# Kernel optimization log

Measured on AMD Instinct MI355X. Metric: run time of the kernel, lower is better.

## Reference

```python
import jax, jax.numpy as jnp
import numpy as np

D_MODEL = 1024
HEADS = 16
HEAD_DIM = D_MODEL // HEADS


def setup_inputs() -> dict:
    key = jax.random.key(0)
    ks = jax.random.split(key, 11)
    B, S = 2, 2048
    scale = 1.0 / np.sqrt(D_MODEL)
    inp = {
        "Q": jax.random.normal(ks[0], (B, S, D_MODEL), jnp.float32),
        "K": jax.random.normal(ks[1], (B, S, D_MODEL), jnp.float32),
        "V": jax.random.normal(ks[2], (B, S, D_MODEL), jnp.float32),
        "Wq": jax.random.normal(ks[3], (D_MODEL, D_MODEL), jnp.float32) * scale,
        "bq": jnp.zeros((D_MODEL,), jnp.float32),
        "Wk": jax.random.normal(ks[4], (D_MODEL, D_MODEL), jnp.float32) * scale,
        "bk": jnp.zeros((D_MODEL,), jnp.float32),
        "Wv": jax.random.normal(ks[5], (D_MODEL, D_MODEL), jnp.float32) * scale,
        "bv": jnp.zeros((D_MODEL,), jnp.float32),
        "Wo": jax.random.normal(ks[6], (D_MODEL, D_MODEL), jnp.float32) * scale,
        "bo": jnp.zeros((D_MODEL,), jnp.float32),
    }
    return inp


def reference(Q, K, V, Wq, bq, Wk, bk, Wv, bv, Wo, bo):
    B, S, _ = Q.shape
    # Linear projections (nn.Linear: x @ W^T + b), split into heads: [B, H, S, Dh]
    def proj(x, W, b):
        y = x @ W.T + b
        return y.reshape(B, S, HEADS, HEAD_DIM).transpose(0, 2, 1, 3)

    q = proj(Q, Wq, bq)
    k = proj(K, Wk, bk)
    v = proj(V, Wv, bv)

    # Scaled dot-product attention (dropout is identity in eval / p=0)
    scores = jnp.einsum("bhqd,bhkd->bhqk", q, k) / jnp.sqrt(
        jnp.asarray(HEAD_DIM, q.dtype)
    )
    weights = jax.nn.softmax(scores, axis=-1)
    ctx = jnp.einsum("bhqk,bhkd->bhqd", weights, v)  # [B, H, S, Dh]

    # Concatenate heads and output projection
    concat = ctx.transpose(0, 2, 1, 3).reshape(B, S, D_MODEL)
    return concat @ Wo.T + bo
```

## Files before the change

kernel.cpp:

```cpp
#include <hip/hip_runtime.h>
#include <hip/hip_bf16.h>

#define D_MODEL 1024
#define HEADS 16
#define HDIM 64
#define BATCH 2
#define SEQ 2048
#define MROWS (BATCH*SEQ)

typedef __attribute__((ext_vector_type(8))) short bf16x8;
typedef __attribute__((ext_vector_type(4))) float f32x4;
typedef __attribute__((ext_vector_type(16))) float f32x16;
typedef __attribute__((ext_vector_type(4))) float float4v;
typedef __attribute__((ext_vector_type(4))) unsigned u32x4;
typedef __attribute__((ext_vector_type(4))) short s16x4;

typedef const __attribute__((address_space(1))) void gconst_t;
typedef __attribute__((address_space(3))) void lds_t;
#define GLD16(g, l) __builtin_amdgcn_global_load_lds((gconst_t*)(g), (lds_t*)(l), 16, 0, 0)

__device__ __forceinline__ unsigned short f2b(float f) {
  unsigned u = __builtin_bit_cast(unsigned, f);
  u += 0x7fffu + ((u >> 16) & 1u);
  return (unsigned short)(u >> 16);
}

__device__ __forceinline__ unsigned cvtpk(float lo, float hi) {
  unsigned r;
  asm volatile("v_cvt_pk_bf16_f32 %0, %1, %2" : "=v"(r) : "v"(lo), "v"(hi));
  return r;
}

__global__ __launch_bounds__(256)
void cast_all(const float* __restrict__ Q, const float* __restrict__ K,
              const float* __restrict__ V, const float* __restrict__ Wq,
              const float* __restrict__ Wk, const float* __restrict__ Wv,
              const float* __restrict__ Wo, char* __restrict__ ws)
{
  const size_t MB = 1024*1024;
  int b = blockIdx.x;
  const float* src; short* dst; int rb;
  if (b < 6144) {
    int t = b >> 11; rb = b & 2047;
    src = (t == 0) ? Q : (t == 1) ? K : V;
    dst = (short*)(ws + (size_t)t*8*MB);
  } else {
    int t = (b - 6144) >> 9; rb = (b - 6144) & 511;
    src = (t == 0) ? Wq : (t == 1) ? Wk : (t == 2) ? Wv : Wo;
    dst = (short*)(ws + (24 + 2*(size_t)t)*MB);
  }
  int i = rb*256 + threadIdx.x;
  const float4v* s = (const float4v*)src;
  float4v a = s[2*(size_t)i], c = s[2*(size_t)i + 1];
  bf16x8 o;
  o[0] = (short)f2b(a[0]); o[1] = (short)f2b(a[1]);
  o[2] = (short)f2b(a[2]); o[3] = (short)f2b(a[3]);
  o[4] = (short)f2b(c[0]); o[5] = (short)f2b(c[1]);
  o[6] = (short)f2b(c[2]); o[7] = (short)f2b(c[3]);
  *(bf16x8*)(dst + 8*(size_t)i) = o;
}

__global__ __launch_bounds__(256)
void gemm_qkv(const short* __restrict__ Qb, const short* __restrict__ Kb,
              const short* __restrict__ Vb, const short* __restrict__ Wqb,
              const short* __restrict__ Wkb, const short* __restrict__ Wvb,
              const float* __restrict__ bq, const float* __restrict__ bk,
              const float* __restrict__ bv, short* __restrict__ qp,
              short* __restrict__ kp, short* __restrict__ vp)
{
  __shared__ __align__(16) short smem[128*129];
  short* lA = smem;
  short* lB = smem + 128*32;
  short* lT = smem;

  const int z = blockIdx.z;
  const short* A = (z == 0) ? Qb : (z == 1) ? Kb : Vb;
  const short* W = (z == 0) ? Wqb : (z == 1) ? Wkb : Wvb;
  const float* bias = (z == 0) ? bq : (z == 1) ? bk : bv;

  const int tid  = threadIdx.x;
  const int wid  = tid >> 6;
  const int lane = tid & 63;
  const int bm = blockIdx.x, bn = blockIdx.y;
  const int wr = wid >> 1, wc = wid & 1;

  f32x4 acc[4][4] = {};

  const int srow = tid >> 2;
  const int sseg = (tid & 3) * 8;
  const short* gA = A + (size_t)(bm*128 + srow)*D_MODEL + sseg;
  const short* gB = W + (size_t)(bn*128 + srow)*D_MODEL + sseg;
  short* lA0 = &lA[(wid*16)*32];
  short* lA1 = &lA[(64 + wid*16)*32];
  short* lB0 = &lB[(wid*16)*32];
  short* lB1 = &lB[(64 + wid*16)*32];

  const int fro  = lane & 15;
  const int koff = (lane >> 4) * 8;

  for (int kt = 0; kt < D_MODEL/32; ++kt) {
    const int ko = kt*32;
    GLD16(gA + ko,               lA0);
    GLD16(gA + 64*D_MODEL + ko,  lA1);
    GLD16(gB + ko,               lB0);
    GLD16(gB + 64*D_MODEL + ko,  lB1);
    __syncthreads();
    bf16x8 af[4], bfv[4];
    #pragma unroll
    for (int i = 0; i < 4; ++i)
      af[i] = *(const bf16x8*)&lA[(wr*64 + i*16 + fro)*32 + koff];
    #pragma unroll
    for (int j = 0; j < 4; ++j)
      bfv[j] = *(const bf16x8*)&lB[(wc*64 + j*16 + fro)*32 + koff];
    #pragma unroll
    for (int i = 0; i < 4; ++i)
      #pragma unroll
      for (int j = 0; j < 4; ++j)
        acc[i][j] = __builtin_amdgcn_mfma_f32_16x16x32_bf16(af[i], bfv[j], acc[i][j], 0, 0, 0);
    __syncthreads();
  }

  if (z < 2) {
    const float sc = (z == 0) ? 0.125f*1.44269504f : 1.0f;
    short* out = (z == 0) ? qp : kp;
    #pragma unroll
    for (int i = 0; i < 4; ++i) {
      #pragma unroll
      for (int r = 0; r < 4; ++r) {
        const int m = bm*128 + wr*64 + i*16 + (lane>>4)*4 + r;
        const int b = m >> 11, s = m & (SEQ-1);
        #pragma unroll
        for (int j = 0; j < 4; ++j) {
          const int n = bn*128 + wc*64 + j*16 + fro;
          const int h = n >> 6, dh = n & 63;
          float v = (acc[i][j][r] + bias[n]) * sc;
          out[((size_t)(b*HEADS + h)*SEQ + s)*HDIM + dh] = (short)f2b(v);
        }
      }
    }
  } else {
    #pragma unroll
    for (int i = 0; i < 4; ++i) {
      #pragma unroll
      for (int r = 0; r < 4; ++r) {
        const int ml = wr*64 + i*16 + (lane>>4)*4 + r;
        #pragma unroll
        for (int j = 0; j < 4; ++j) {
          const int nl = wc*64 + j*16 + fro;
          lT[nl*129 + ml] = (short)f2b(acc[i][j][r] + bias[bn*128 + nl]);
        }
      }
    }
    __syncthreads();
    const int nl = tid >> 1, mh = (tid & 1) * 64;
    const int n = bn*128 + nl, h = n >> 6, dh = n & 63;
    const int b  = (bm*128) >> 11;
    const int s0 = (bm*128) & (SEQ-1);
    const size_t base = ((size_t)(b*HEADS + h)*HDIM + dh)*SEQ + s0 + mh;
    #pragma unroll
    for (int v8 = 0; v8 < 8; ++v8) {
      bf16x8 vv;
      #pragma unroll
      for (int e = 0; e < 8; ++e) vv[e] = lT[nl*129 + mh + v8*8 + e];
      *(bf16x8*)&vp[base + v8*8] = vv;
    }
  }
}

__global__ __launch_bounds__(256)
void gemm_out(const short* __restrict__ A, const short* __restrict__ W,
              const float* __restrict__ bias, float* __restrict__ out)
{
  __shared__ __align__(16) short lA[128*32];
  __shared__ __align__(16) short lB[128*32];

  const int tid  = threadIdx.x;
  const int wid  = tid >> 6;
  const int lane = tid & 63;
  const int bm = blockIdx.x, bn = blockIdx.y;
  const int wr = wid >> 1, wc = wid & 1;

  f32x4 acc[4][4] = {};
  const int srow = tid >> 2;
  const int sseg = (tid & 3) * 8;
  const short* gA = A + (size_t)(bm*128 + srow)*D_MODEL + sseg;
  const short* gB = W + (size_t)(bn*128 + srow)*D_MODEL + sseg;
  short* lA0 = &lA[(wid*16)*32];
  short* lA1 = &lA[(64 + wid*16)*32];
  short* lB0 = &lB[(wid*16)*32];
  short* lB1 = &lB[(64 + wid*16)*32];
  const int fro  = lane & 15;
  const int koff = (lane >> 4) * 8;

  for (int kt = 0; kt < D_MODEL/32; ++kt) {
    const int ko = kt*32;
    GLD16(gA + ko,               lA0);
    GLD16(gA + 64*D_MODEL + ko,  lA1);
    GLD16(gB + ko,               lB0);
    GLD16(gB + 64*D_MODEL + ko,  lB1);
    __syncthreads();
    bf16x8 af[4], bfv[4];
    #pragma unroll
    for (int i = 0; i < 4; ++i)
      af[i] = *(const bf16x8*)&lA[(wr*64 + i*16 + fro)*32 + koff];
    #pragma unroll
    for (int j = 0; j < 4; ++j)
      bfv[j] = *(const bf16x8*)&lB[(wc*64 + j*16 + fro)*32 + koff];
    #pragma unroll
    for (int i = 0; i < 4; ++i)
      #pragma unroll
      for (int j = 0; j < 4; ++j)
        acc[i][j] = __builtin_amdgcn_mfma_f32_16x16x32_bf16(af[i], bfv[j], acc[i][j], 0, 0, 0);
    __syncthreads();
  }

  #pragma unroll
  for (int i = 0; i < 4; ++i) {
    #pragma unroll
    for (int r = 0; r < 4; ++r) {
      const int m = bm*128 + wr*64 + i*16 + (lane>>4)*4 + r;
      #pragma unroll
      for (int j = 0; j < 4; ++j) {
        const int n = bn*128 + wc*64 + j*16 + fro;
        out[(size_t)m*D_MODEL + n] = acc[i][j][r] + bias[n];
      }
    }
  }
}

__global__ __launch_bounds__(512)
void attn(const short* __restrict__ qws, const short* __restrict__ kws,
          const short* __restrict__ vws, short* __restrict__ ctx)
{
  __shared__ __align__(16) short lK[2][2][64*64];
  __shared__ __align__(16) short lV[2][2][64*64];

  const int tid = threadIdx.x, wid = tid >> 6, lane = tid & 63;
  const int sw = wid & 3, half = wid >> 2;
  const int bid = blockIdx.x;
  const int wg = (bid & 7) * 64 + (bid >> 3);
  const int qt = wg & 15, bh = wg >> 4;
  const size_t hb = (size_t)bh * SEQ * HDIM;

  const int lane31 = lane & 31, hi = lane >> 5;
  const int tidl = sw*64 + lane;
  const int tr0  = tidl >> 3;
  const int cswz = (((tidl & 7) * 16) ^ ((tr0 & 7) << 4)) >> 1;

  const short* gK = kws + hb;
  const short* gV = vws + hb;

#define STAGEKV(t, bb) do { \
    GLD16(gK + (size_t)((t)*64 + tr0)*HDIM + cswz,      &lK[half][bb][(sw*8)*64]); \
    GLD16(gK + (size_t)((t)*64 + 32 + tr0)*HDIM + cswz, &lK[half][bb][(32+sw*8)*64]); \
    GLD16(gV + (size_t)tr0*SEQ + (t)*64 + cswz,         &lV[half][bb][(sw*8)*64]); \
    GLD16(gV + (size_t)(32+tr0)*SEQ + (t)*64 + cswz,    &lV[half][bb][(32+sw*8)*64]); \
  } while (0)

  const int kt0 = half * 16;
  STAGEKV(kt0, 0);

  const int q = qt*128 + sw*32 + lane31;
  const short* gq = qws + hb + (size_t)q*HDIM + hi*8;
  bf16x8 qf[4];
  #pragma unroll
  for (int ks = 0; ks < 4; ++ks) qf[ks] = *(const bf16x8*)(gq + ks*16);

  f32x16 o0 = {}, o1 = {};
  float lrow = 0.f;
  const int swz = (lane31 & 7) << 4;

  __syncthreads();

  for (int k2 = 0; k2 < 16; ++k2) {
    const short* Kc = &lK[half][k2 & 1][0];
    const short* Vc = &lV[half][k2 & 1][0];
    if (k2 + 1 < 16) STAGEKV(kt0 + k2 + 1, (k2 + 1) & 1);

    #pragma unroll
    for (int kb = 0; kb < 2; ++kb) {
      f32x16 s = {};
      __builtin_amdgcn_s_setprio(1);
      #pragma unroll
      for (int ks = 0; ks < 4; ++ks) {
        bf16x8 kf = *(const bf16x8*)&Kc[(kb*32 + lane31)*64 + (((ks*32 + hi*16) ^ swz) >> 1)];
        s = __builtin_amdgcn_mfma_f32_32x32x16_bf16(kf, qf[ks], s, 0, 0, 0);
      }
      __builtin_amdgcn_s_setprio(0);

      float p[16]; float rs = 0.f;
      #pragma unroll
      for (int r = 0; r < 16; ++r) { p[r] = __builtin_exp2f(s[r]); rs += p[r]; }
      lrow += rs;

      unsigned w0 = cvtpk(p[0],  p[1]),  w1 = cvtpk(p[2],  p[3]);
      unsigned w2 = cvtpk(p[4],  p[5]),  w3 = cvtpk(p[6],  p[7]);
      unsigned w4 = cvtpk(p[8],  p[9]),  w5 = cvtpk(p[10], p[11]);
      unsigned w6 = cvtpk(p[12], p[13]), w7 = cvtpk(p[14], p[15]);
      unsigned y0 = hi ? w0 : w2, y1 = hi ? w1 : w3;
      unsigned y2 = hi ? w4 : w6, y3 = hi ? w5 : w7;
      unsigned z0 = (unsigned)__shfl_xor((int)y0, 32);
      unsigned z1 = (unsigned)__shfl_xor((int)y1, 32);
      unsigned z2 = (unsigned)__shfl_xor((int)y2, 32);
      unsigned z3 = (unsigned)__shfl_xor((int)y3, 32);
      u32x4 pw0 = { hi ? z0 : w0, hi ? z1 : w1, hi ? w2 : z0, hi ? w3 : z1 };
      u32x4 pw1 = { hi ? z2 : w4, hi ? z3 : w5, hi ? w6 : z2, hi ? w7 : z3 };
      bf16x8 pa0 = __builtin_bit_cast(bf16x8, pw0);
      bf16x8 pa1 = __builtin_bit_cast(bf16x8, pw1);

      __builtin_amdgcn_s_setprio(1);
      #pragma unroll
      for (int ksl = 0; ksl < 2; ++ksl) {
        const int vcol = ((kb*64 + ksl*32 + hi*16) ^ swz) >> 1;
        bf16x8 pav = ksl ? pa1 : pa0;
        bf16x8 vf0 = *(const bf16x8*)&Vc[lane31*64 + vcol];
        bf16x8 vf1 = *(const bf16x8*)&Vc[(32 + lane31)*64 + vcol];
        o0 = __builtin_amdgcn_mfma_f32_32x32x16_bf16(vf0, pav, o0, 0, 0, 0);
        o1 = __builtin_amdgcn_mfma_f32_32x32x16_bf16(vf1, pav, o1, 0, 0, 0);
      }
      __builtin_amdgcn_s_setprio(0);
    }
    __syncthreads();
  }

  lrow += __shfl_xor(lrow, 32);

  float* xo = (float*)&lK[0][0][0];
  float* xl = (float*)&lV[0][0][0];
  if (half == 1) {
    #pragma unroll
    for (int g = 0; g < 4; ++g) {
      #pragma unroll
      for (int e = 0; e < 4; ++e) {
        const int dh = g*8 + hi*4 + e;
        xo[sw*2048 + dh*32 + lane31]        = o0[g*4 + e];
        xo[sw*2048 + (32 + dh)*32 + lane31] = o1[g*4 + e];
      }
    }
    if (hi == 0) xl[sw*32 + lane31] = lrow;
  }
  __syncthreads();
  if (half == 0) {
    const float inv = 1.0f / (lrow + xl[sw*32 + lane31]);
    const int b_ = bh >> 4, h_ = bh & (HEADS-1);
    const size_t base = ((size_t)(b_*SEQ) + q)*D_MODEL + h_*HDIM;
    #pragma unroll
    for (int g = 0; g < 4; ++g) {
      s16x4 pk0, pk1;
      #pragma unroll
      for (int e = 0; e < 4; ++e) {
        const int dh = g*8 + hi*4 + e;
        pk0[e] = (short)f2b((o0[g*4+e] + xo[sw*2048 + dh*32 + lane31]) * inv);
        pk1[e] = (short)f2b((o1[g*4+e] + xo[sw*2048 + (32+dh)*32 + lane31]) * inv);
      }
      *(s16x4*)&ctx[base +      g*8 + hi*4] = pk0;
      *(s16x4*)&ctx[base + 32 + g*8 + hi*4] = pk1;
    }
  }
#undef STAGEKV
}

extern "C" void kernel_launch(void* const* d_in, const int* in_sizes, int n_in,
                              void* d_out, int out_size, void* d_ws, size_t ws_size,
                              hipStream_t stream)
{
  const float* Q  = (const float*)d_in[0];
  const float* K  = (const float*)d_in[1];
  const float* V  = (const float*)d_in[2];
  const float* Wq = (const float*)d_in[3];
  const float* bq = (const float*)d_in[4];
  const float* Wk = (const float*)d_in[5];
  const float* bk = (const float*)d_in[6];
  const float* Wv = (const float*)d_in[7];
  const float* bv = (const float*)d_in[8];
  const float* Wo = (const float*)d_in[9];
  const float* bo = (const float*)d_in[10];

  char* ws = (char*)d_ws;
  const size_t MB = 1024*1024;
  short* Qb  = (short*)(ws +  0*MB);
  short* Kb  = (short*)(ws +  8*MB);
  short* Vb  = (short*)(ws + 16*MB);
  short* Wqb = (short*)(ws + 24*MB);
  short* Wkb = (short*)(ws + 26*MB);
  short* Wvb = (short*)(ws + 28*MB);
  short* Wob = (short*)(ws + 30*MB);
  short* qp  = (short*)(ws + 32*MB);
  short* kp  = (short*)(ws + 40*MB);
  short* vp  = (short*)(ws + 48*MB);
  short* cx  = (short*)(ws + 56*MB);

  cast_all<<<8192, 256, 0, stream>>>(Q, K, V, Wq, Wk, Wv, Wo, ws);
  gemm_qkv<<<dim3(MROWS/128, D_MODEL/128, 3), 256, 0, stream>>>(
      Qb, Kb, Vb, Wqb, Wkb, Wvb, bq, bk, bv, qp, kp, vp);
  attn<<<512, 512, 0, stream>>>(qp, kp, vp, cx);
  gemm_out<<<dim3(MROWS/128, D_MODEL/128), 256, 0, stream>>>(cx, Wob, bo, (float*)d_out);
}
```

Measured before the change: 148.2 us.

## Widen GEMM K-tile to 64 with XOR-swizzled LDS and use native exp2

```diff
diff --git a/kernel.cpp b/kernel.cpp
--- a/kernel.cpp
+++ b/kernel.cpp
@@ -18,6 +18,12 @@
 typedef const __attribute__((address_space(1))) void gconst_t;
 typedef __attribute__((address_space(3))) void lds_t;
 #define GLD16(g, l) __builtin_amdgcn_global_load_lds((gconst_t*)(g), (lds_t*)(l), 16, 0, 0)
+
+#if __has_builtin(__builtin_amdgcn_exp2f)
+#define EXP2(x) __builtin_amdgcn_exp2f(x)
+#else
+#define EXP2(x) __builtin_exp2f(x)
+#endif
 
 __device__ __forceinline__ unsigned short f2b(float f) {
   unsigned u = __builtin_bit_cast(unsigned, f);
@@ -70,7 +76,7 @@
 {
   __shared__ __align__(16) short smem[128*129];
   short* lA = smem;
-  short* lB = smem + 128*32;
+  short* lB = smem + 128*64;
   short* lT = smem;
 
   const int z = blockIdx.z;
@@ -86,37 +92,51 @@
 
   f32x4 acc[4][4] = {};
 
-  const int srow = tid >> 2;
-  const int sseg = (tid & 3) * 8;
-  const short* gA = A + (size_t)(bm*128 + srow)*D_MODEL + sseg;
-  const short* gB = W + (size_t)(bn*128 + srow)*D_MODEL + sseg;
-  short* lA0 = &lA[(wid*16)*32];
-  short* lA1 = &lA[(64 + wid*16)*32];
-  short* lB0 = &lB[(wid*16)*32];
-  short* lB1 = &lB[(64 + wid*16)*32];
-
-  const int fro  = lane & 15;
-  const int koff = (lane >> 4) * 8;
-
-  for (int kt = 0; kt < D_MODEL/32; ++kt) {
-    const int ko = kt*32;
+  const int srow = tid >> 3;
+  const int cswz = (((tid & 7) * 16) ^ ((srow & 7) << 4)) >> 1;
+  const short* gA = A + (size_t)(bm*128 + srow)*D_MODEL + cswz;
+  const short* gB = W + (size_t)(bn*128 + srow)*D_MODEL + cswz;
+  short* lA0 = &lA[(     wid*8)*64];
+  short* lA1 = &lA[(32 + wid*8)*64];
+  short* lA2 = &lA[(64 + wid*8)*64];
+  short* lA3 = &lA[(96 + wid*8)*64];
+  short* lB0 = &lB[(     wid*8)*64];
+  short* lB1 = &lB[(32 + wid*8)*64];
+  short* lB2 = &lB[(64 + wid*8)*64];
+  short* lB3 = &lB[(96 + wid*8)*64];
+
+  const int fro = lane & 15;
+  const int xr7 = (fro & 7) << 4;
+  const int c0  = ((((lane >> 4) << 4))      ^ xr7) >> 1;
+  const int c1  = ((64 + ((lane >> 4) << 4)) ^ xr7) >> 1;
+
+  for (int kt = 0; kt < D_MODEL/64; ++kt) {
+    const int ko = kt*64;
     GLD16(gA + ko,               lA0);
-    GLD16(gA + 64*D_MODEL + ko,  lA1);
+    GLD16(gA + 32*D_MODEL + ko,  lA1);
+    GLD16(gA + 64*D_MODEL + ko,  lA2);
+    GLD16(gA + 96*D_MODEL + ko,  lA3);
     GLD16(gB + ko,               lB0);
-    GLD16(gB + 64*D_MODEL + ko,  lB1);
-    __syncthreads();
-    bf16x8 af[4], bfv[4];
-    #pragma unroll
-    for (int i = 0; i < 4; ++i)
-      af[i] = *(const bf16x8*)&lA[(wr*64 + i*16 + fro)*32 + koff];
-    #pragma unroll
-    for (int j = 0; j < 4; ++j)
-      bfv[j] = *(const bf16x8*)&lB[(wc*64 + j*16 + fro)*32 + koff];
-    #pragma unroll
-    for (int i = 0; i < 4; ++i)
+    GLD16(gB + 32*D_MODEL + ko,  lB1);
+    GLD16(gB + 64*D_MODEL + ko,  lB2);
+    GLD16(gB + 96*D_MODEL + ko,  lB3);
+    __syncthreads();
+    #pragma unroll
+    for (int ks2 = 0; ks2 < 2; ++ks2) {
+      const int cc = ks2 ? c1 : c0;
+      bf16x8 af[4], bfv[4];
+      #pragma unroll
+      for (int i = 0; i < 4; ++i)
+        af[i] = *(const bf16x8*)&lA[(wr*64 + i*16 + fro)*64 + cc];
       #pragma unroll
       for (int j = 0; j < 4; ++j)
-        acc[i][j] = __builtin_amdgcn_mfma_f32_16x16x32_bf16(af[i], bfv[j], acc[i][j], 0, 0, 0);
+        bfv[j] = *(const bf16x8*)&lB[(wc*64 + j*16 + fro)*64 + cc];
+      #pragma unroll
+      for (int i = 0; i < 4; ++i)
+        #pragma unroll
+        for (int j = 0; j < 4; ++j)
+          acc[i][j] = __builtin_amdgcn_mfma_f32_16x16x32_bf16(af[i], bfv[j], acc[i][j], 0, 0, 0);
+    }
     __syncthreads();
   }
 
@@ -171,8 +191,8 @@
 void gemm_out(const short* __restrict__ A, const short* __restrict__ W,
               const float* __restrict__ bias, float* __restrict__ out)
 {
-  __shared__ __align__(16) short lA[128*32];
-  __shared__ __align__(16) short lB[128*32];
+  __shared__ __align__(16) short lA[128*64];
+  __shared__ __align__(16) short lB[128*64];
 
   const int tid  = threadIdx.x;
   const int wid  = tid >> 6;
@@ -181,36 +201,51 @@
   const int wr = wid >> 1, wc = wid & 1;
 
   f32x4 acc[4][4] = {};
-  const int srow = tid >> 2;
-  const int sseg = (tid & 3) * 8;
-  const short* gA = A + (size_t)(bm*128 + srow)*D_MODEL + sseg;
-  const short* gB = W + (size_t)(bn*128 + srow)*D_MODEL + sseg;
-  short* lA0 = &lA[(wid*16)*32];
-  short* lA1 = &lA[(64 + wid*16)*32];
-  short* lB0 = &lB[(wid*16)*32];
-  short* lB1 = &lB[(64 + wid*16)*32];
-  const int fro  = lane & 15;
-  const int koff = (lane >> 4) * 8;
-
-  for (int kt = 0; kt < D_MODEL/32; ++kt) {
-    const int ko = kt*32;
+  const int srow = tid >> 3;
+  const int cswz = (((tid & 7) * 16) ^ ((srow & 7) << 4)) >> 1;
+  const short* gA = A + (size_t)(bm*128 + srow)*D_MODEL + cswz;
+  const short* gB = W + (size_t)(bn*128 + srow)*D_MODEL + cswz;
+  short* lA0 = &lA[(     wid*8)*64];
+  short* lA1 = &lA[(32 + wid*8)*64];
+  short* lA2 = &lA[(64 + wid*8)*64];
+  short* lA3 = &lA[(96 + wid*8)*64];
+  short* lB0 = &lB[(     wid*8)*64];
+  short* lB1 = &lB[(32 + wid*8)*64];
+  short* lB2 = &lB[(64 + wid*8)*64];
+  short* lB3 = &lB[(96 + wid*8)*64];
+
+  const int fro = lane & 15;
+  const int xr7 = (fro & 7) << 4;
+  const int c0  = ((((lane >> 4) << 4))      ^ xr7) >> 1;
+  const int c1  = ((64 + ((lane >> 4) << 4)) ^ xr7) >> 1;
+
+  for (int kt = 0; kt < D_MODEL/64; ++kt) {
+    const int ko = kt*64;
     GLD16(gA + ko,               lA0);
-    GLD16(gA + 64*D_MODEL + ko,  lA1);
+    GLD16(gA + 32*D_MODEL + ko,  lA1);
+    GLD16(gA + 64*D_MODEL + ko,  lA2);
+    GLD16(gA + 96*D_MODEL + ko,  lA3);
     GLD16(gB + ko,               lB0);
-    GLD16(gB + 64*D_MODEL + ko,  lB1);
-    __syncthreads();
-    bf16x8 af[4], bfv[4];
-    #pragma unroll
-    for (int i = 0; i < 4; ++i)
-      af[i] = *(const bf16x8*)&lA[(wr*64 + i*16 + fro)*32 + koff];
-    #pragma unroll
-    for (int j = 0; j < 4; ++j)
-      bfv[j] = *(const bf16x8*)&lB[(wc*64 + j*16 + fro)*32 + koff];
-    #pragma unroll
-    for (int i = 0; i < 4; ++i)
+    GLD16(gB + 32*D_MODEL + ko,  lB1);
+    GLD16(gB + 64*D_MODEL + ko,  lB2);
+    GLD16(gB + 96*D_MODEL + ko,  lB3);
+    __syncthreads();
+    #pragma unroll
+    for (int ks2 = 0; ks2 < 2; ++ks2) {
+      const int cc = ks2 ? c1 : c0;
+      bf16x8 af[4], bfv[4];
+      #pragma unroll
+      for (int i = 0; i < 4; ++i)
+        af[i] = *(const bf16x8*)&lA[(wr*64 + i*16 + fro)*64 + cc];
       #pragma unroll
       for (int j = 0; j < 4; ++j)
-        acc[i][j] = __builtin_amdgcn_mfma_f32_16x16x32_bf16(af[i], bfv[j], acc[i][j], 0, 0, 0);
+        bfv[j] = *(const bf16x8*)&lB[(wc*64 + j*16 + fro)*64 + cc];
+      #pragma unroll
+      for (int i = 0; i < 4; ++i)
+        #pragma unroll
+        for (int j = 0; j < 4; ++j)
+          acc[i][j] = __builtin_amdgcn_mfma_f32_16x16x32_bf16(af[i], bfv[j], acc[i][j], 0, 0, 0);
+    }
     __syncthreads();
   }
 
@@ -290,7 +325,7 @@
 
       float p[16]; float rs = 0.f;
       #pragma unroll
-      for (int r = 0; r < 16; ++r) { p[r] = __builtin_exp2f(s[r]); rs += p[r]; }
+      for (int r = 0; r < 16; ++r) { p[r] = EXP2(s[r]); rs += p[r]; }
       lrow += rs;
 
       unsigned w0 = cvtpk(p[0],  p[1]),  w1 = cvtpk(p[2],  p[3]);
```

New measurement: 129.6 us. -12.5%, faster.
